# Optimization experiments

Hardware: AMD Instinct MI355X
Metric: run time of the kernel (lower is better)

The kernel has to match this reference:

```python
import jax, jax.numpy as jnp
import numpy as np

N_NODES = 100000
N_EDGES = 3200000
N_ELEMS = 10


def setup_inputs() -> dict:
    key = jax.random.key(0)
    k1, k2, k3, k4, k5 = jax.random.split(key, 5)
    # edge distances in (0.1, 5.1) Angstrom, shape [E, 1]
    x = jax.random.uniform(k1, (N_EDGES, 1), dtype=jnp.float32) * 5.0 + 0.1
    # one-hot-ish node element encoding; only argmax matters
    node_attrs = jax.random.normal(k2, (N_NODES, N_ELEMS), dtype=jnp.float32)
    edge_index = jax.random.randint(k3, (2, N_EDGES), 0, N_NODES)
    # atomic numbers of the chemical species present (1..89)
    atomic_numbers = jax.random.randint(k4, (N_ELEMS,), 1, 90)
    # stand-in for ase.data.covalent_radii (119 entries, ~0.3..2.3 A)
    covalent_radii = jax.random.uniform(k5, (119,), dtype=jnp.float32) * 2.0 + 0.3
    return {
        "x": x,
        "node_attrs": node_attrs,
        "edge_index": edge_index,
        "atomic_numbers": atomic_numbers,
        "covalent_radii": covalent_radii,
    }


def _polynomial_envelope(x, r_max, p):
    # PolynomialCutoff.calculate_envelope, p = 6
    r = x / r_max
    env = (1.0
           - (p + 1.0) * (p + 2.0) / 2.0 * jnp.power(r, p)
           + p * (p + 2.0) * jnp.power(r, p + 1)
           - p * (p + 1.0) / 2.0 * jnp.power(r, p + 2))
    return env * (x < r_max)


def reference(x, node_attrs, edge_index, atomic_numbers, covalent_radii):
    c = jnp.array([0.1818, 0.5099, 0.2802, 0.02817], dtype=jnp.float32)
    p = 6.0
    a_exp = jnp.float32(0.3)
    a_prefactor = jnp.float32(0.4543)

    sender, receiver = edge_index[0], edge_index[1]
    # per-node atomic number from one-hot attrs, [N, 1]
    node_Z = atomic_numbers[jnp.argmax(node_attrs, axis=1)][..., None]
    Z_u = node_Z[sender].astype(jnp.int32)  # [E, 1]
    Z_v = node_Z[receiver].astype(jnp.int32)  # [E, 1]
    Zu_f = Z_u.astype(jnp.float32)
    Zv_f = Z_v.astype(jnp.float32)

    a = a_prefactor * 0.529 / (jnp.power(Zu_f, a_exp) + jnp.power(Zv_f, a_exp))
    r_over_a = x / a  # [E, 1]
    phi = (c[0] * jnp.exp(-3.2 * r_over_a)
           + c[1] * jnp.exp(-0.9423 * r_over_a)
           + c[2] * jnp.exp(-0.4028 * r_over_a)
           + c[3] * jnp.exp(-0.2016 * r_over_a))
    v_edges = 14.3996 * Zu_f * Zv_f / x * phi  # [E, 1]

    r_max = covalent_radii[Z_u] + covalent_radii[Z_v]  # [E, 1]
    envelope = _polynomial_envelope(x, r_max, p)
    v_edges = 0.5 * v_edges * envelope  # [E, 1]

    # scatter-sum edge energies into receiver nodes -> [N]
    V_ZBL = jax.ops.segment_sum(v_edges[:, 0], receiver,
                                num_segments=node_attrs.shape[0])
    return V_ZBL
```

## Files before the change

kernel.cpp:

```cpp
#include <hip/hip_runtime.h>
#include <stdint.h>

#define N_NODES 100000
#define N_ELEM4 50000
#define N_EDGES 3200000
#define N_ELEMS 10
#define N_PAIRS (N_ELEMS * N_ELEMS)

#define NB 256
#define NPB 391
#define SCAT_THREADS 1024
#define NBLK 512
#define EPB 6256
#define NGROUPS (EPB / 4)
#define NG4 (N_EDGES / 4)
#define PREP_BLOCKS 196

#define CAP 24
#define REC_PER_B (NBLK * CAP)
#define OVF_CAP 16384

#define L_ELEM  0
#define L_TAB   50000
#define L_CNT   (L_TAB + 1600)
#define L_REC   (L_CNT + 1024)
#define LDS_BYTES (L_REC + NB * CAP * 4)

__global__ __launch_bounds__(256) void prep_kernel(
    const float* __restrict__ node_attrs,
    const int* __restrict__ atomic_numbers,
    const float* __restrict__ covalent_radii,
    uint8_t* __restrict__ node_elem4,
    float4* __restrict__ pair_tab,
    unsigned int* __restrict__ ovf_cnt) {
  int i = blockIdx.x * 256 + threadIdx.x;

  if (blockIdx.x == 0) {
    if (threadIdx.x < N_PAIRS) {
      int t = threadIdx.x;
      int eu = t / N_ELEMS, ev = t % N_ELEMS;
      float Zuf = (float)atomic_numbers[eu];
      float Zvf = (float)atomic_numbers[ev];
      float a = 0.4543f * 0.529f / (powf(Zuf, 0.3f) + powf(Zvf, 0.3f));
      float rmax = covalent_radii[(int)Zuf] + covalent_radii[(int)Zvf];
      pair_tab[t] = make_float4(1.0f / a, 0.5f * 14.3996f * Zuf * Zvf,
                                rmax, 1.0f / rmax);
    }
    if (threadIdx.x == 0) *ovf_cnt = 0u;
  }

  if (i < N_ELEM4) {
    unsigned int packed = 0;
#pragma unroll
    for (int h = 0; h < 2; ++h) {
      int node = 2 * i + h;
      const float2* row = (const float2*)(node_attrs + (size_t)node * N_ELEMS);
      float best = -INFINITY;
      int bj = 0;
#pragma unroll
      for (int k = 0; k < 5; ++k) {
        float2 v = row[k];
        if (v.x > best) { best = v.x; bj = 2 * k; }
        if (v.y > best) { best = v.y; bj = 2 * k + 1; }
      }
      packed |= (unsigned int)bj << (h * 4);
    }
    node_elem4[i] = (uint8_t)packed;
  }
}

__device__ __forceinline__ float edge_val(float xi, int u, int v,
                                          const uint8_t* s_elem4,
                                          const float4* s_tab) {
  int eu = (s_elem4[u >> 1] >> ((u & 1) * 4)) & 0xF;
  int ev = (s_elem4[v >> 1] >> ((v & 1) * 4)) & 0xF;
  float4 tb = s_tab[eu * N_ELEMS + ev];
  float roa = xi * tb.x;
  float phi = 0.1818f  * __expf(-3.2f    * roa)
            + 0.5099f  * __expf(-0.9423f * roa)
            + 0.2802f  * __expf(-0.4028f * roa)
            + 0.02817f * __expf(-0.2016f * roa);
  float val = tb.y * phi * __builtin_amdgcn_rcpf(xi);
  float r  = xi * tb.w;
  float r2 = r * r;
  float r6 = r2 * r2 * r2;
  float env = 1.0f - 28.0f * r6 + 48.0f * r6 * r - 21.0f * r6 * r2;
  return (xi < tb.z) ? val * env : 0.0f;
}

__global__ __launch_bounds__(SCAT_THREADS) void scatter_kernel(
    const float* __restrict__ x,
    const int* __restrict__ edge_index,
    const uint8_t* __restrict__ node_elem4,
    const float4* __restrict__ pair_tab,
    unsigned int* __restrict__ records,
    unsigned int* __restrict__ ovf_cnt,
    uint2* __restrict__ ovf) {
  extern __shared__ char smem[];
  uint4*        s_elem4_v = (uint4*)(smem + L_ELEM);
  float4*       s_tab     = (float4*)(smem + L_TAB);
  unsigned int* s_cnt     = (unsigned int*)(smem + L_CNT);
  unsigned int* s_rec     = (unsigned int*)(smem + L_REC);
  const uint8_t* s_elem4  = (const uint8_t*)s_elem4_v;

  int tid = threadIdx.x;

  {
    const uint4* src = (const uint4*)node_elem4;
    for (int j = tid; j < N_ELEM4 / 16; j += SCAT_THREADS) s_elem4_v[j] = src[j];
  }
  if (tid < N_PAIRS) s_tab[tid] = pair_tab[tid];
  if (tid < NB) s_cnt[tid] = 0u;
  __syncthreads();

#pragma unroll
  for (int k = 0; k < 2; ++k) {
    int gl = k * SCAT_THREADS + tid;
    int g  = blockIdx.x * NGROUPS + gl;
    if (gl >= NGROUPS || g >= NG4) continue;
    int e = g * 4;
    float4 xv = *(const float4*)(x + e);
    int4 uu = *(const int4*)(edge_index + e);
    int4 vv = *(const int4*)(edge_index + N_EDGES + e);
    int ru[4] = {uu.x, uu.y, uu.z, uu.w};
    int rv[4] = {vv.x, vv.y, vv.z, vv.w};
    float xs[4] = {xv.x, xv.y, xv.z, xv.w};
#pragma unroll
    for (int c = 0; c < 4; ++c) {
      float v = edge_val(xs[c], ru[c], rv[c], s_elem4, s_tab);
      if (v != 0.0f) {
        unsigned int b = (unsigned int)rv[c] / NPB;
        unsigned int lid = (unsigned int)rv[c] - b * NPB;
        unsigned int r = atomicAdd(&s_cnt[b], 1u);
        if (r < CAP) {
          s_rec[b * CAP + r] = (__float_as_uint(v) & ~0x1FFu) | lid;
        } else {
          unsigned int idx = atomicAdd(ovf_cnt, 1u);
          if (idx < OVF_CAP)
            ovf[idx] = make_uint2(__float_as_uint(v), (unsigned int)rv[c]);
        }
      }
    }
  }
  __syncthreads();

  for (int j = tid; j < NB * CAP; j += SCAT_THREADS) {
    int b = j / CAP, slot = j - b * CAP;
    unsigned int c = s_cnt[b]; if (c > CAP) c = CAP;
    unsigned int rec = ((unsigned int)slot < c) ? s_rec[j] : 0u;
    records[(size_t)b * REC_PER_B + (size_t)blockIdx.x * CAP + slot] = rec;
  }
}

__global__ __launch_bounds__(1024) void reduce_kernel(
    const unsigned int* __restrict__ records,
    const unsigned int* __restrict__ ovf_cnt,
    const uint2* __restrict__ ovf,
    float* __restrict__ out) {
  __shared__ float bins[NPB];
  int b = blockIdx.x, tid = threadIdx.x;

  if (tid < NPB) bins[tid] = 0.0f;
  __syncthreads();

  const unsigned int* rp = records + (size_t)b * REC_PER_B;
  for (int i = tid; i < REC_PER_B; i += 1024) {
    unsigned int rec = rp[i];
    if (rec != 0u)
      atomicAdd(&bins[rec & 0x1FFu], __uint_as_float(rec & ~0x1FFu));
  }

  unsigned int on = *ovf_cnt; if (on > OVF_CAP) on = OVF_CAP;
  for (unsigned int j = tid; j < on; j += 1024) {
    uint2 e2 = ovf[j];
    unsigned int nb = e2.y / NPB;
    if (nb == (unsigned int)b)
      atomicAdd(&bins[e2.y - nb * NPB], __uint_as_float(e2.x));
  }
  __syncthreads();

  int nb0 = b * NPB;
  if (tid < NPB && nb0 + tid < N_NODES) out[nb0 + tid] = bins[tid];
}

extern "C" void kernel_launch(void* const* d_in, const int* in_sizes, int n_in,
                              void* d_out, int out_size, void* d_ws, size_t ws_size,
                              hipStream_t stream) {
  const float* x              = (const float*)d_in[0];
  const float* node_attrs     = (const float*)d_in[1];
  const int*   edge_index     = (const int*)d_in[2];
  const int*   atomic_numbers = (const int*)d_in[3];
  const float* covalent_radii = (const float*)d_in[4];
  float* out = (float*)d_out;

  char* wsp = (char*)d_ws;
  unsigned int* records    = (unsigned int*)wsp;
  unsigned int* ovf_cnt    = (unsigned int*)(wsp + 12582912);
  uint2*        ovf        = (uint2*)(wsp + 12582928);
  float4*       pair_tab   = (float4*)(wsp + 12714000);
  uint8_t*      node_elem4 = (uint8_t*)(wsp + 12715600);

  prep_kernel<<<PREP_BLOCKS, 256, 0, stream>>>(
      node_attrs, atomic_numbers, covalent_radii, node_elem4, pair_tab,
      ovf_cnt);

  scatter_kernel<<<NBLK, SCAT_THREADS, LDS_BYTES, stream>>>(
      x, edge_index, node_elem4, pair_tab, records, ovf_cnt, ovf);

  reduce_kernel<<<NB, 1024, 0, stream>>>(records, ovf_cnt, ovf, out);
}
```

Before: 104.4 us.

## Fuse scatter and reduce kernels with a global atomic grid barrier

Merges the separate reduce kernel into the scatter kernel. Every block increments a global counter after writing its records, and the last 256 blocks spin on that counter until all 512 blocks have arrived before reducing one bin range each. This removes one kernel launch and its inter-kernel gap. It relies on all 512 blocks being co-resident, since the spin-wait deadlocks otherwise, and blocks that finish early sit idle while they wait.

After: 145.4 us. 39.3% more time.

```diff
diff --git a/kernel.cpp b/kernel.cpp
--- a/kernel.cpp
+++ b/kernel.cpp
@@ -9,7 +9,7 @@
 
 #define NB 256
 #define NPB 391
-#define SCAT_THREADS 1024
+#define THREADS 1024
 #define NBLK 512
 #define EPB 6256
 #define NGROUPS (EPB / 4)
@@ -32,7 +32,7 @@
     const float* __restrict__ covalent_radii,
     uint8_t* __restrict__ node_elem4,
     float4* __restrict__ pair_tab,
-    unsigned int* __restrict__ ovf_cnt) {
+    unsigned int* __restrict__ ctrs) {
   int i = blockIdx.x * 256 + threadIdx.x;
 
   if (blockIdx.x == 0) {
@@ -46,7 +46,7 @@
       pair_tab[t] = make_float4(1.0f / a, 0.5f * 14.3996f * Zuf * Zvf,
                                 rmax, 1.0f / rmax);
     }
-    if (threadIdx.x == 0) *ovf_cnt = 0u;
+    if (threadIdx.x == 0) { ctrs[0] = 0u; ctrs[1] = 0u; }
   }
 
   if (i < N_ELEM4) {
@@ -88,26 +88,29 @@
   return (xi < tb.z) ? val * env : 0.0f;
 }
 
-__global__ __launch_bounds__(SCAT_THREADS) void scatter_kernel(
+__global__ __launch_bounds__(THREADS, 8) void scatter_reduce_kernel(
     const float* __restrict__ x,
     const int* __restrict__ edge_index,
     const uint8_t* __restrict__ node_elem4,
     const float4* __restrict__ pair_tab,
     unsigned int* __restrict__ records,
-    unsigned int* __restrict__ ovf_cnt,
-    uint2* __restrict__ ovf) {
+    unsigned int* __restrict__ ctrs,
+    uint2* __restrict__ ovf,
+    float* __restrict__ out) {
   extern __shared__ char smem[];
   uint4*        s_elem4_v = (uint4*)(smem + L_ELEM);
   float4*       s_tab     = (float4*)(smem + L_TAB);
   unsigned int* s_cnt     = (unsigned int*)(smem + L_CNT);
   unsigned int* s_rec     = (unsigned int*)(smem + L_REC);
   const uint8_t* s_elem4  = (const uint8_t*)s_elem4_v;
+  unsigned int* ovf_cnt = ctrs;
+  unsigned int* bar     = ctrs + 1;
 
   int tid = threadIdx.x;
 
   {
     const uint4* src = (const uint4*)node_elem4;
-    for (int j = tid; j < N_ELEM4 / 16; j += SCAT_THREADS) s_elem4_v[j] = src[j];
+    for (int j = tid; j < N_ELEM4 / 16; j += THREADS) s_elem4_v[j] = src[j];
   }
   if (tid < N_PAIRS) s_tab[tid] = pair_tab[tid];
   if (tid < NB) s_cnt[tid] = 0u;
@@ -115,7 +118,7 @@
 
 #pragma unroll
   for (int k = 0; k < 2; ++k) {
-    int gl = k * SCAT_THREADS + tid;
+    int gl = k * THREADS + tid;
     int g  = blockIdx.x * NGROUPS + gl;
     if (gl >= NGROUPS || g >= NG4) continue;
     int e = g * 4;
@@ -144,43 +147,55 @@
   }
   __syncthreads();
 
-  for (int j = tid; j < NB * CAP; j += SCAT_THREADS) {
+  for (int j = tid; j < NB * CAP; j += THREADS) {
     int b = j / CAP, slot = j - b * CAP;
     unsigned int c = s_cnt[b]; if (c > CAP) c = CAP;
     unsigned int rec = ((unsigned int)slot < c) ? s_rec[j] : 0u;
     records[(size_t)b * REC_PER_B + (size_t)blockIdx.x * CAP + slot] = rec;
   }
-}
-
-__global__ __launch_bounds__(1024) void reduce_kernel(
-    const unsigned int* __restrict__ records,
-    const unsigned int* __restrict__ ovf_cnt,
-    const uint2* __restrict__ ovf,
-    float* __restrict__ out) {
-  __shared__ float bins[NPB];
-  int b = blockIdx.x, tid = threadIdx.x;
-
-  if (tid < NPB) bins[tid] = 0.0f;
-  __syncthreads();
-
-  const unsigned int* rp = records + (size_t)b * REC_PER_B;
-  for (int i = tid; i < REC_PER_B; i += 1024) {
-    unsigned int rec = rp[i];
-    if (rec != 0u)
-      atomicAdd(&bins[rec & 0x1FFu], __uint_as_float(rec & ~0x1FFu));
-  }
-
-  unsigned int on = *ovf_cnt; if (on > OVF_CAP) on = OVF_CAP;
-  for (unsigned int j = tid; j < on; j += 1024) {
-    uint2 e2 = ovf[j];
-    unsigned int nb = e2.y / NPB;
-    if (nb == (unsigned int)b)
-      atomicAdd(&bins[e2.y - nb * NPB], __uint_as_float(e2.x));
-  }
-  __syncthreads();
-
-  int nb0 = b * NPB;
-  if (tid < NPB && nb0 + tid < N_NODES) out[nb0 + tid] = bins[tid];
+
+  __syncthreads();
+  if (tid == 0) {
+    __threadfence();
+    __hip_atomic_fetch_add(bar, 1u, __ATOMIC_RELEASE,
+                           __HIP_MEMORY_SCOPE_AGENT);
+  }
+  if (blockIdx.x < (NBLK - NB)) return;
+
+  if (tid == 0) {
+    while (__hip_atomic_load(bar, __ATOMIC_RELAXED,
+                             __HIP_MEMORY_SCOPE_AGENT) < NBLK)
+      __builtin_amdgcn_s_sleep(2);
+    __threadfence();
+  }
+  __syncthreads();
+
+  {
+    float* bins = (float*)smem;
+    int b = blockIdx.x - (NBLK - NB);
+
+    if (tid < NPB) bins[tid] = 0.0f;
+    __syncthreads();
+
+    const unsigned int* rp = records + (size_t)b * REC_PER_B;
+    for (int i = tid; i < REC_PER_B; i += THREADS) {
+      unsigned int rec = rp[i];
+      if (rec != 0u)
+        atomicAdd(&bins[rec & 0x1FFu], __uint_as_float(rec & ~0x1FFu));
+    }
+
+    unsigned int on = *ovf_cnt; if (on > OVF_CAP) on = OVF_CAP;
+    for (unsigned int j = tid; j < on; j += THREADS) {
+      uint2 e2 = ovf[j];
+      unsigned int nb = e2.y / NPB;
+      if (nb == (unsigned int)b)
+        atomicAdd(&bins[e2.y - nb * NPB], __uint_as_float(e2.x));
+    }
+    __syncthreads();
+
+    int nb0 = b * NPB;
+    if (tid < NPB && nb0 + tid < N_NODES) out[nb0 + tid] = bins[tid];
+  }
 }
 
 extern "C" void kernel_launch(void* const* d_in, const int* in_sizes, int n_in,
@@ -195,17 +210,14 @@
 
   char* wsp = (char*)d_ws;
   unsigned int* records    = (unsigned int*)wsp;
-  unsigned int* ovf_cnt    = (unsigned int*)(wsp + 12582912);
+  unsigned int* ctrs       = (unsigned int*)(wsp + 12582912);
   uint2*        ovf        = (uint2*)(wsp + 12582928);
   float4*       pair_tab   = (float4*)(wsp + 12714000);
   uint8_t*      node_elem4 = (uint8_t*)(wsp + 12715600);
 
   prep_kernel<<<PREP_BLOCKS, 256, 0, stream>>>(
-      node_attrs, atomic_numbers, covalent_radii, node_elem4, pair_tab,
-      ovf_cnt);
-
-  scatter_kernel<<<NBLK, SCAT_THREADS, LDS_BYTES, stream>>>(
-      x, edge_index, node_elem4, pair_tab, records, ovf_cnt, ovf);
-
-  reduce_kernel<<<NB, 1024, 0, stream>>>(records, ovf_cnt, ovf, out);
-}
+      node_attrs, atomic_numbers, covalent_radii, node_elem4, pair_tab, ctrs);
+
+  scatter_reduce_kernel<<<NBLK, THREADS, LDS_BYTES, stream>>>(
+      x, edge_index, node_elem4, pair_tab, records, ctrs, ovf, out);
+}
```
